# Performance work log

Measured on AMD Instinct MI355X. Metric: run time of the kernel, lower is better.

## Reference

```python
import jax, jax.numpy as jnp
import numpy as np

B, S, D, DQKV = 4, 2048, 1024, 1024

def setup_inputs() -> dict:
    key = jax.random.key(0)
    kx, kq, kk, kv = jax.random.split(key, 4)
    scale = 1.0 / np.sqrt(D)
    return {
        "x": jax.random.normal(kx, (B, S, D), dtype=jnp.float32),
        "wq": jax.random.normal(kq, (D, DQKV), dtype=jnp.float32) * scale,
        "wk": jax.random.normal(kk, (D, DQKV), dtype=jnp.float32) * scale,
        "wv": jax.random.normal(kv, (D, DQKV), dtype=jnp.float32) * scale,
    }

def reference(x, wq, wk, wv):
    # QKV projections: [B,S,D] @ [D,Dqkv] -> [B,S,Dqkv]
    q = jnp.einsum('bsd,de->bse', x, wq)
    k = jnp.einsum('bsd,de->bse', x, wk)
    v = jnp.einsum('bsd,de->bse', x, wv)
    # scores: [B,S,S], scaled by sqrt(dim_qkv)
    scores = jnp.einsum('bik,bjk->bij', q, k) / jnp.sqrt(jnp.asarray(DQKV, dtype=x.dtype))
    attn = jax.nn.softmax(scores, axis=-1)
    # output: [B,S,Dqkv]
    return jnp.einsum('bij,bjd->bid', attn, v)
```

## Files before the change

kernel.cpp:

```cpp
#include <hip/hip_runtime.h>
#include <cstdint>
#include <cstddef>

typedef __bf16 bf16;
typedef __bf16 bf16x4 __attribute__((ext_vector_type(4)));
typedef __bf16 bf16x8 __attribute__((ext_vector_type(8)));
typedef float  f32x4  __attribute__((ext_vector_type(4)));
typedef float  f32x16 __attribute__((ext_vector_type(16)));

#define BATCH 4
#define SEQ   2048
#define DIM   1024
#define LDP   2112

__device__ __forceinline__ bf16 to_bf16(float f) {
    unsigned u = __builtin_bit_cast(unsigned, f);
    u += 0x7fffu + ((u >> 16) & 1u);
    unsigned short h = (unsigned short)(u >> 16);
    return __builtin_bit_cast(bf16, h);
}

__device__ __forceinline__ void load16_lds(const bf16* g, bf16* l) {
    __builtin_amdgcn_global_load_lds(
        (__attribute__((address_space(1))) void*)(g),
        (__attribute__((address_space(3))) void*)(l),
        16, 0, 0);
}

#define BARRIER() do { asm volatile("" ::: "memory"); \
                       __builtin_amdgcn_s_barrier();  \
                       asm volatile("" ::: "memory"); } while (0)
#define LGKM0()   asm volatile("s_waitcnt lgkmcnt(0)" ::: "memory")
#define VM4()     asm volatile("s_waitcnt vmcnt(4)" ::: "memory")
#define VM0()     asm volatile("s_waitcnt vmcnt(0)" ::: "memory")


__device__ __forceinline__ void stage_half(
    const bf16* __restrict__ srcRow0, int ld, int k0, bf16* dstHalfBase)
{
    const int tid  = threadIdx.x;
    const int wave = tid >> 6;
    const int lane = tid & 63;
    const int rg   = lane >> 3;
    const int scoff = ((lane & 7) ^ rg) * 8;
#pragma unroll
    for (int j = 0; j < 2; ++j) {
        const int r = wave * 16 + j * 8;
        load16_lds(srcRow0 + (size_t)(r + rg) * ld + k0 + scoff,
                   dstHalfBase + r * 64);
    }
}

template<int MB, int NB>
__device__ __forceinline__ void mfma_quad(
    const bf16x8 a[4][2], const bf16x8 b[4][2], f32x4 acc[8][4])
{
    __builtin_amdgcn_s_setprio(1);
#pragma unroll
    for (int m = 0; m < 4; ++m)
#pragma unroll
        for (int n = 0; n < 2; ++n)
#pragma unroll
            for (int ks = 0; ks < 2; ++ks)
                acc[MB + m][NB + n] = __builtin_amdgcn_mfma_f32_16x16x32_bf16(
                    a[m][ks], b[NB + n][ks], acc[MB + m][NB + n], 0, 0, 0);
    __builtin_amdgcn_s_setprio(0);
}

__device__ __forceinline__ void gemm8_core(
    const bf16* __restrict__ Ablk, const bf16* __restrict__ Bblk,
    int K, int lda, int ldb, bf16* As, bf16* Bs, f32x4 acc[8][4])
{
    const int tid  = threadIdx.x;
    const int lane = tid & 63;
    const int wave = tid >> 6;
    const int wr   = wave >> 2;
    const int wc   = wave & 3;
    const int r16  = lane & 15;
    const int g    = lane >> 4;
    const int r7   = r16 & 7;
    const int pk0  = ((g) ^ r7) * 8;
    const int pk1  = ((4 + g) ^ r7) * 8;
    const int arow = (wr * 128 + r16) * 64;
    const int brow = (wc * 64 + r16) * 64;
    const int NT   = K >> 6;

    stage_half(Bblk, ldb, 0, Bs);
    stage_half(Ablk, lda, 0, As);
    stage_half(Bblk + (size_t)128 * ldb, ldb, 0, Bs + 8192);
    stage_half(Ablk + (size_t)128 * lda, lda, 0, As + 8192);
    stage_half(Bblk, ldb, 64, Bs + 16384);
    stage_half(Ablk, lda, 64, As + 16384);
    VM4();
    BARRIER();

    bf16x8 a[4][2], b[4][2];
#pragma unroll 2
    for (int t = 0; t < NT; ++t) {
        bf16* Ac = As + (t & 1) * 16384;
        bf16* Bc = Bs + (t & 1) * 16384;
        bf16* An = As + ((t + 1) & 1) * 16384;
        bf16* Bn = Bs + ((t + 1) & 1) * 16384;
        const int k1 = (t + 1) << 6;
        const int k2 = (t + 2) << 6;

#pragma unroll
        for (int m = 0; m < 4; ++m) {
            a[m][0] = *(const bf16x8*)(Ac + arow + m * 1024 + pk0);
            a[m][1] = *(const bf16x8*)(Ac + arow + m * 1024 + pk1);
        }
#pragma unroll
        for (int n = 0; n < 2; ++n) {
            b[n][0] = *(const bf16x8*)(Bc + brow + n * 1024 + pk0);
            b[n][1] = *(const bf16x8*)(Bc + brow + n * 1024 + pk1);
        }
        if (t + 1 < NT) stage_half(Bblk + (size_t)128 * ldb, ldb, k1, Bn + 8192);
        BARRIER(); LGKM0();
        mfma_quad<0, 0>(a, b, acc);
        BARRIER();

#pragma unroll
        for (int n = 2; n < 4; ++n) {
            b[n][0] = *(const bf16x8*)(Bc + brow + n * 1024 + pk0);
            b[n][1] = *(const bf16x8*)(Bc + brow + n * 1024 + pk1);
        }
        if (t + 1 < NT) stage_half(Ablk + (size_t)128 * lda, lda, k1, An + 8192);
        BARRIER(); LGKM0();
        mfma_quad<0, 2>(a, b, acc);
        BARRIER();

#pragma unroll
        for (int m = 0; m < 4; ++m) {
            a[m][0] = *(const bf16x8*)(Ac + arow + 4096 + m * 1024 + pk0);
            a[m][1] = *(const bf16x8*)(Ac + arow + 4096 + m * 1024 + pk1);
        }
        if (t + 2 < NT) stage_half(Bblk, ldb, k2, Bc);
        BARRIER(); LGKM0();
        mfma_quad<4, 2>(a, b, acc);
        BARRIER();

        if (t + 2 < NT) stage_half(Ablk, lda, k2, Ac);
        BARRIER(); LGKM0();
        mfma_quad<4, 0>(a, b, acc);
        if (t + 1 < NT) {
            if (t + 2 < NT) { VM4(); } else { VM0(); }
        }
        BARRIER();
    }
}

__device__ __forceinline__ void stage_tiles(
    const bf16* __restrict__ Abase, const bf16* __restrict__ Bbase,
    int k0, int lda, int ldb, bf16* As, bf16* Bs)
{
    const int tid   = threadIdx.x;
    const int wave  = tid >> 6;
    const int lane  = tid & 63;
    const int srow0 = wave * 8 + (lane >> 3);
    const int scoff = (((lane & 7) ^ ((lane >> 3) & 7)) * 8);
    const int ldsW  = wave * 512;
#pragma unroll
    for (int j = 0; j < 4; ++j) {
        load16_lds(Abase + (size_t)(j * 32 + srow0) * lda + k0 + scoff,
                   As + j * 2048 + ldsW);
        load16_lds(Bbase + (size_t)(j * 32 + srow0) * ldb + k0 + scoff,
                   Bs + j * 2048 + ldsW);
    }
}

__device__ __forceinline__ void gemm_core64_32(
    const bf16* __restrict__ Abase, const bf16* __restrict__ Bbase,
    int K, int lda, int ldb, bf16* As, bf16* Bs, f32x16 acc[2][2])
{
    const int tid  = threadIdx.x;
    const int lane = tid & 63;
    const int wave = tid >> 6;
    const int wm   = (wave >> 1) * 64;
    const int wn   = (wave & 1) * 64;
    const int r32  = lane & 31;
    const int hi   = lane >> 5;

    for (int k0 = 0; k0 < K; k0 += 64) {
        __syncthreads();
        stage_tiles(Abase, Bbase, k0, lda, ldb, As, Bs);
        __syncthreads();
#pragma unroll
        for (int t = 0; t < 4; ++t) {
            bf16x8 af[2], bfr[2];
            const int p = (2 * t + hi) ^ (r32 & 7);
#pragma unroll
            for (int i = 0; i < 2; ++i) {
                af[i]  = *(const bf16x8*)(As + (wm + i * 32 + r32) * 64 + p * 8);
                bfr[i] = *(const bf16x8*)(Bs + (wn + i * 32 + r32) * 64 + p * 8);
            }
#pragma unroll
            for (int mi = 0; mi < 2; ++mi)
#pragma unroll
                for (int ni = 0; ni < 2; ++ni)
                    acc[mi][ni] = __builtin_amdgcn_mfma_f32_32x32x16_bf16(
                        af[mi], bfr[ni], acc[mi][ni], 0, 0, 0);
        }
    }
}

__device__ __forceinline__ int c32_row(int reg, int hi) {
    return (reg & 3) + 8 * (reg >> 2) + 4 * hi;
}

__global__ __launch_bounds__(512, 2) void proj_gemm8(
    const bf16* __restrict__ xb, const bf16* __restrict__ Wt,
    bf16* __restrict__ Q, bf16* __restrict__ Kb, bf16* __restrict__ Vt)
{
    __shared__ bf16 As[32768];
    __shared__ bf16 Bs[32768];
    f32x4 acc[8][4] = {};

    const int r = blockIdx.x;
    const bf16 *Ab, *Bb;
    bf16* Cb;
    int ldc;
    if (r < 256) {
        const int my = r >> 3, j = r & 7;
        Ab = xb + (size_t)my * 256 * DIM;
        Bb = Wt + (size_t)((j >> 2) ? DIM * DIM : 0) + (size_t)(j & 3) * 256 * DIM;
        bf16* dst = (j >> 2) ? Kb : Q;
        Cb = dst + (size_t)my * 256 * DIM + (size_t)(j & 3) * 256;
        ldc = DIM;
    } else {
        const int u = r - 256;
        const int bz = u >> 5, w = u & 31;
        const int vy = w >> 3, vx = w & 7;
        Ab = Wt + (size_t)2 * DIM * DIM + (size_t)vy * 256 * DIM;
        Bb = xb + (size_t)bz * SEQ * DIM + (size_t)vx * 256 * DIM;
        Cb = Vt + (size_t)bz * DIM * LDP + (size_t)vy * 256 * LDP + (size_t)vx * 256;
        ldc = LDP;
    }
    gemm8_core(Ab, Bb, DIM, DIM, DIM, As, Bs, acc);

    const int lane = threadIdx.x & 63;
    const int wave = threadIdx.x >> 6;
    const int wr = wave >> 2, wc = wave & 3;
    const int r16 = lane & 15, g = lane >> 4;
    const int row0 = wr * 128 + g * 4;
    const int col0 = wc * 64 + r16;
#pragma unroll
    for (int m = 0; m < 8; ++m)
#pragma unroll
        for (int n = 0; n < 4; ++n)
#pragma unroll
            for (int rr = 0; rr < 4; ++rr)
                Cb[(size_t)(row0 + m * 16 + rr) * ldc + col0 + n * 16] =
                    to_bf16(acc[m][n][rr]);
}

__global__ __launch_bounds__(512, 2) void gemm_scores8(
    const bf16* __restrict__ Qm, const bf16* __restrict__ Kb,
    bf16* __restrict__ P, float* __restrict__ lsum)
{
    __shared__ bf16 As[32768];
    __shared__ bf16 Bs[32768];
    f32x4 acc[8][4] = {};

    const int d = blockIdx.x;
    const int bx = d & 7, by = (d >> 3) & 7, bz = d >> 6;
    const bf16* Ab = Qm + (size_t)bz * SEQ * DIM + (size_t)by * 256 * DIM;
    const bf16* Bb = Kb + (size_t)bz * SEQ * DIM + (size_t)bx * 256 * DIM;
    gemm8_core(Ab, Bb, DIM, DIM, DIM, As, Bs, acc);

    bf16* Cb  = P + (size_t)bz * SEQ * LDP;
    float* ls = lsum + (size_t)bz * SEQ;
    const int lane = threadIdx.x & 63;
    const int wave = threadIdx.x >> 6;
    const int wr = wave >> 2, wc = wave & 3;
    const int r16 = lane & 15, g = lane >> 4;
    const int rowB = by * 256 + wr * 128 + g * 4;
    const int colB = bx * 256 + wc * 64 + r16;
#pragma unroll
    for (int m = 0; m < 8; ++m)
#pragma unroll
        for (int rr = 0; rr < 4; ++rr) {
            float s = 0.0f;
#pragma unroll
            for (int n = 0; n < 4; ++n) {
                const float e = __expf(acc[m][n][rr] * 0.03125f);
                s += e;
                Cb[(size_t)(rowB + m * 16 + rr) * LDP + colB + n * 16] = to_bf16(e);
            }
            s += __shfl_xor(s, 1);
            s += __shfl_xor(s, 2);
            s += __shfl_xor(s, 4);
            s += __shfl_xor(s, 8);
            if (r16 == 0)
                atomicAdd(ls + rowB + m * 16 + rr, s);
        }
}

__global__ __launch_bounds__(256, 4) void gemm_pv(
    const bf16* __restrict__ P, const bf16* __restrict__ Vt, float* __restrict__ C,
    const float* __restrict__ lsum)
{
    __shared__ bf16 As[8192];
    __shared__ bf16 Bs[8192];
    f32x16 acc[2][2] = {};

    const int d = blockIdx.x + 8 * (blockIdx.y + 16 * blockIdx.z);
    const int c = d & 7, j = d >> 3;
    const int bx = j & 7;
    const int p = c + 8 * (j >> 3);
    const int by = p & 15, bz = p >> 4;

    const bf16* Ab = P  + (size_t)bz * SEQ * LDP + (size_t)by * 128 * LDP;
    const bf16* Bb = Vt + (size_t)bz * DIM * LDP + (size_t)bx * 128 * LDP;
    float* Cb = C + (size_t)bz * SEQ * DIM;
    gemm_core64_32(Ab, Bb, SEQ, LDP, LDP, As, Bs, acc);

    const int lane = threadIdx.x & 63;
    const int wave = threadIdx.x >> 6;
    const int hi = lane >> 5, r32 = lane & 31;
    const int wm = (wave >> 1) * 64, wn = (wave & 1) * 64;
    const int rowBase = by * 128 + wm;
    const int colBase = bx * 128 + wn + r32;
    const float* ls = lsum + (size_t)bz * SEQ;
#pragma unroll
    for (int mi = 0; mi < 2; ++mi)
#pragma unroll
        for (int reg = 0; reg < 16; ++reg) {
            const int row = rowBase + mi * 32 + c32_row(reg, hi);
            const float inv = __builtin_amdgcn_rcpf(ls[row]);
#pragma unroll
            for (int ni = 0; ni < 2; ++ni)
                Cb[(size_t)row * DIM + colBase + ni * 32] = acc[mi][ni][reg] * inv;
        }
}

__global__ __launch_bounds__(256) void prep(
    const float* __restrict__ x,  const float* __restrict__ wq,
    const float* __restrict__ wk, const float* __restrict__ wv,
    bf16* __restrict__ xb, bf16* __restrict__ Wt, float* __restrict__ lsum)
{
    __shared__ float tile[32][33];
    const int b = blockIdx.x;
    const int tid = threadIdx.x;
    if (b < 8192) {
        const size_t i = ((size_t)b * 256 + tid) * 4;
        const float4 v = *(const float4*)(x + i);
        bf16x4 o = { to_bf16(v.x), to_bf16(v.y), to_bf16(v.z), to_bf16(v.w) };
        *(bf16x4*)(xb + i) = o;
    } else if (b < 8192 + 3072) {
        const int t   = b - 8192;
        const int sel = t >> 10;
        const int n0  = (t & 31) * 32;
        const int k0  = ((t >> 5) & 31) * 32;
        const float* w = (sel == 0) ? wq : (sel == 1) ? wk : wv;
        const int tx = tid & 31, ty = tid >> 5;
#pragma unroll
        for (int j = 0; j < 32; j += 8)
            tile[ty + j][tx] = w[(size_t)(k0 + ty + j) * 1024 + n0 + tx];
        __syncthreads();
        bf16* dst = Wt + (size_t)sel * 1024 * 1024;
#pragma unroll
        for (int j = 0; j < 32; j += 8)
            dst[(size_t)(n0 + ty + j) * 1024 + k0 + tx] = to_bf16(tile[tx][ty + j]);
    } else {
#pragma unroll
        for (int i = 0; i < 32; ++i)
            lsum[i * 256 + tid] = 0.0f;
    }
}

extern "C" void kernel_launch(void* const* d_in, const int* in_sizes, int n_in,
                              void* d_out, int out_size, void* d_ws, size_t ws_size,
                              hipStream_t stream)
{
    const float* x  = (const float*)d_in[0];
    const float* wq = (const float*)d_in[1];
    const float* wk = (const float*)d_in[2];
    const float* wv = (const float*)d_in[3];
    float* out = (float*)d_out;
    char* ws = (char*)d_ws;

    bf16*  xb   = (bf16*)(ws);
    bf16*  Wt   = (bf16*)(ws + (16u << 20));
    bf16*  Q    = (bf16*)(ws + (22u << 20));
    bf16*  Kb   = (bf16*)(ws + (38u << 20));
    bf16*  Vt   = (bf16*)(ws + (54u << 20));
    bf16*  P    = (bf16*)(ws + (72u << 20));
    float* lsum = (float*)(ws + (108u << 20));

    prep<<<dim3(8192 + 3072 + 1), dim3(256), 0, stream>>>(
        x, wq, wk, wv, xb, Wt, lsum);

    proj_gemm8<<<dim3(384), dim3(512), 0, stream>>>(xb, Wt, Q, Kb, Vt);

    gemm_scores8<<<dim3(256), dim3(512), 0, stream>>>(Q, Kb, P, lsum);

    gemm_pv<<<dim3(8, 16, 4), dim3(256), 0, stream>>>(P, Vt, out, lsum);
}
```

Baseline: 245.8 us.

## Replace 8-wave ping-pong GEMM schedule with simple double-buffered loop, split projection launch

```diff
diff --git a/kernel.cpp b/kernel.cpp
--- a/kernel.cpp
+++ b/kernel.cpp
@@ -31,7 +31,6 @@
                        __builtin_amdgcn_s_barrier();  \
                        asm volatile("" ::: "memory"); } while (0)
 #define LGKM0()   asm volatile("s_waitcnt lgkmcnt(0)" ::: "memory")
-#define VM4()     asm volatile("s_waitcnt vmcnt(4)" ::: "memory")
 #define VM0()     asm volatile("s_waitcnt vmcnt(0)" ::: "memory")
 
 
@@ -51,23 +50,7 @@
     }
 }
 
-template<int MB, int NB>
-__device__ __forceinline__ void mfma_quad(
-    const bf16x8 a[4][2], const bf16x8 b[4][2], f32x4 acc[8][4])
-{
-    __builtin_amdgcn_s_setprio(1);
-#pragma unroll
-    for (int m = 0; m < 4; ++m)
-#pragma unroll
-        for (int n = 0; n < 2; ++n)
-#pragma unroll
-            for (int ks = 0; ks < 2; ++ks)
-                acc[MB + m][NB + n] = __builtin_amdgcn_mfma_f32_16x16x32_bf16(
-                    a[m][ks], b[NB + n][ks], acc[MB + m][NB + n], 0, 0, 0);
-    __builtin_amdgcn_s_setprio(0);
-}
-
-__device__ __forceinline__ void gemm8_core(
+__device__ __forceinline__ void gemm_big_core(
     const bf16* __restrict__ Ablk, const bf16* __restrict__ Bblk,
     int K, int lda, int ldb, bf16* As, bf16* Bs, f32x4 acc[8][4])
 {
@@ -86,15 +69,12 @@
     const int NT   = K >> 6;
 
     stage_half(Bblk, ldb, 0, Bs);
+    stage_half(Bblk + (size_t)128 * ldb, ldb, 0, Bs + 8192);
     stage_half(Ablk, lda, 0, As);
-    stage_half(Bblk + (size_t)128 * ldb, ldb, 0, Bs + 8192);
     stage_half(Ablk + (size_t)128 * lda, lda, 0, As + 8192);
-    stage_half(Bblk, ldb, 64, Bs + 16384);
-    stage_half(Ablk, lda, 64, As + 16384);
-    VM4();
+    VM0();
     BARRIER();
 
-    bf16x8 a[4][2], b[4][2];
 #pragma unroll 2
     for (int t = 0; t < NT; ++t) {
         bf16* Ac = As + (t & 1) * 16384;
@@ -102,51 +82,69 @@
         bf16* An = As + ((t + 1) & 1) * 16384;
         bf16* Bn = Bs + ((t + 1) & 1) * 16384;
         const int k1 = (t + 1) << 6;
-        const int k2 = (t + 2) << 6;
-
+
+        bf16x8 b[4][2], a[4][2], a2[4][2];
+#pragma unroll
+        for (int n = 0; n < 4; ++n) {
+            b[n][0] = *(const bf16x8*)(Bc + brow + n * 1024 + pk0);
+            b[n][1] = *(const bf16x8*)(Bc + brow + n * 1024 + pk1);
+        }
 #pragma unroll
         for (int m = 0; m < 4; ++m) {
             a[m][0] = *(const bf16x8*)(Ac + arow + m * 1024 + pk0);
             a[m][1] = *(const bf16x8*)(Ac + arow + m * 1024 + pk1);
         }
-#pragma unroll
-        for (int n = 0; n < 2; ++n) {
-            b[n][0] = *(const bf16x8*)(Bc + brow + n * 1024 + pk0);
-            b[n][1] = *(const bf16x8*)(Bc + brow + n * 1024 + pk1);
-        }
-        if (t + 1 < NT) stage_half(Bblk + (size_t)128 * ldb, ldb, k1, Bn + 8192);
-        BARRIER(); LGKM0();
-        mfma_quad<0, 0>(a, b, acc);
+        if (t + 1 < NT) {
+            stage_half(Bblk, ldb, k1, Bn);
+            stage_half(Bblk + (size_t)128 * ldb, ldb, k1, Bn + 8192);
+            stage_half(Ablk, lda, k1, An);
+            stage_half(Ablk + (size_t)128 * lda, lda, k1, An + 8192);
+        }
+#pragma unroll
+        for (int m = 0; m < 4; ++m)
+#pragma unroll
+            for (int n = 0; n < 4; ++n)
+#pragma unroll
+                for (int ks = 0; ks < 2; ++ks)
+                    acc[m][n] = __builtin_amdgcn_mfma_f32_16x16x32_bf16(
+                        a[m][ks], b[n][ks], acc[m][n], 0, 0, 0);
+#pragma unroll
+        for (int m = 0; m < 4; ++m) {
+            a2[m][0] = *(const bf16x8*)(Ac + arow + 4096 + m * 1024 + pk0);
+            a2[m][1] = *(const bf16x8*)(Ac + arow + 4096 + m * 1024 + pk1);
+        }
+#pragma unroll
+        for (int m = 0; m < 4; ++m)
+#pragma unroll
+            for (int n = 0; n < 4; ++n)
+#pragma unroll
+                for (int ks = 0; ks < 2; ++ks)
+                    acc[4 + m][n] = __builtin_amdgcn_mfma_f32_16x16x32_bf16(
+                        a2[m][ks], b[n][ks], acc[4 + m][n], 0, 0, 0);
+
+        LGKM0();
+        if (t + 1 < NT) VM0();
         BARRIER();
-
-#pragma unroll
-        for (int n = 2; n < 4; ++n) {
-            b[n][0] = *(const bf16x8*)(Bc + brow + n * 1024 + pk0);
-            b[n][1] = *(const bf16x8*)(Bc + brow + n * 1024 + pk1);
-        }
-        if (t + 1 < NT) stage_half(Ablk + (size_t)128 * lda, lda, k1, An + 8192);
-        BARRIER(); LGKM0();
-        mfma_quad<0, 2>(a, b, acc);
-        BARRIER();
-
-#pragma unroll
-        for (int m = 0; m < 4; ++m) {
-            a[m][0] = *(const bf16x8*)(Ac + arow + 4096 + m * 1024 + pk0);
-            a[m][1] = *(const bf16x8*)(Ac + arow + 4096 + m * 1024 + pk1);
-        }
-        if (t + 2 < NT) stage_half(Bblk, ldb, k2, Bc);
-        BARRIER(); LGKM0();
-        mfma_quad<4, 2>(a, b, acc);
-        BARRIER();
-
-        if (t + 2 < NT) stage_half(Ablk, lda, k2, Ac);
-        BARRIER(); LGKM0();
-        mfma_quad<4, 0>(a, b, acc);
-        if (t + 1 < NT) {
-            if (t + 2 < NT) { VM4(); } else { VM0(); }
-        }
-        BARRIER();
-    }
+    }
+}
+
+__device__ __forceinline__ void write_c256(
+    bf16* __restrict__ Cb, int ldc, const f32x4 acc[8][4])
+{
+    const int lane = threadIdx.x & 63;
+    const int wave = threadIdx.x >> 6;
+    const int wr = wave >> 2, wc = wave & 3;
+    const int r16 = lane & 15, g = lane >> 4;
+    const int row0 = wr * 128 + g * 4;
+    const int col0 = wc * 64 + r16;
+#pragma unroll
+    for (int m = 0; m < 8; ++m)
+#pragma unroll
+        for (int n = 0; n < 4; ++n)
+#pragma unroll
+            for (int rr = 0; rr < 4; ++rr)
+                Cb[(size_t)(row0 + m * 16 + rr) * ldc + col0 + n * 16] =
+                    to_bf16(acc[m][n][rr]);
 }
 
 __device__ __forceinline__ void stage_tiles(
@@ -207,50 +205,44 @@
     return (reg & 3) + 8 * (reg >> 2) + 4 * hi;
 }
 
-__global__ __launch_bounds__(512, 2) void proj_gemm8(
+__global__ __launch_bounds__(512, 2) void proj_qk(
     const bf16* __restrict__ xb, const bf16* __restrict__ Wt,
-    bf16* __restrict__ Q, bf16* __restrict__ Kb, bf16* __restrict__ Vt)
+    bf16* __restrict__ Q, bf16* __restrict__ Kb)
 {
     __shared__ bf16 As[32768];
     __shared__ bf16 Bs[32768];
     f32x4 acc[8][4] = {};
 
     const int r = blockIdx.x;
-    const bf16 *Ab, *Bb;
-    bf16* Cb;
-    int ldc;
-    if (r < 256) {
-        const int my = r >> 3, j = r & 7;
-        Ab = xb + (size_t)my * 256 * DIM;
-        Bb = Wt + (size_t)((j >> 2) ? DIM * DIM : 0) + (size_t)(j & 3) * 256 * DIM;
-        bf16* dst = (j >> 2) ? Kb : Q;
-        Cb = dst + (size_t)my * 256 * DIM + (size_t)(j & 3) * 256;
-        ldc = DIM;
-    } else {
-        const int u = r - 256;
-        const int bz = u >> 5, w = u & 31;
-        const int vy = w >> 3, vx = w & 7;
-        Ab = Wt + (size_t)2 * DIM * DIM + (size_t)vy * 256 * DIM;
-        Bb = xb + (size_t)bz * SEQ * DIM + (size_t)vx * 256 * DIM;
-        Cb = Vt + (size_t)bz * DIM * LDP + (size_t)vy * 256 * LDP + (size_t)vx * 256;
-        ldc = LDP;
-    }
-    gemm8_core(Ab, Bb, DIM, DIM, DIM, As, Bs, acc);
-
-    const int lane = threadIdx.x & 63;
-    const int wave = threadIdx.x >> 6;
-    const int wr = wave >> 2, wc = wave & 3;
-    const int r16 = lane & 15, g = lane >> 4;
-    const int row0 = wr * 128 + g * 4;
-    const int col0 = wc * 64 + r16;
-#pragma unroll
-    for (int m = 0; m < 8; ++m)
-#pragma unroll
-        for (int n = 0; n < 4; ++n)
-#pragma unroll
-            for (int rr = 0; rr < 4; ++rr)
-                Cb[(size_t)(row0 + m * 16 + rr) * ldc + col0 + n * 16] =
-                    to_bf16(acc[m][n][rr]);
+    const int my = r >> 3, j = r & 7;
+    const bf16* Ab = xb + (size_t)my * 256 * DIM;
+    const bf16* Bb = Wt + (size_t)((j >> 2) ? DIM * DIM : 0)
+                        + (size_t)(j & 3) * 256 * DIM;
+    bf16* dst = (j >> 2) ? Kb : Q;
+    bf16* Cb = dst + (size_t)my * 256 * DIM + (size_t)(j & 3) * 256;
+
+    gemm_big_core(Ab, Bb, DIM, DIM, DIM, As, Bs, acc);
+    write_c256(Cb, DIM, acc);
+}
+
+__global__ __launch_bounds__(512, 2) void proj_v(
+    const bf16* __restrict__ xb, const bf16* __restrict__ Wt,
+    bf16* __restrict__ Vt)
+{
+    __shared__ bf16 As[32768];
+    __shared__ bf16 Bs[32768];
+    f32x4 acc[8][4] = {};
+
+    const int u = blockIdx.x;
+    const int bz = u >> 5, w = u & 31;
+    const int vy = w >> 3, vx = w & 7;
+    const bf16* Ab = Wt + (size_t)2 * DIM * DIM + (size_t)vy * 256 * DIM;
+    const bf16* Bb = xb + (size_t)bz * SEQ * DIM + (size_t)vx * 256 * DIM;
+    bf16* Cb = Vt + (size_t)bz * DIM * LDP + (size_t)vy * 256 * LDP
+                  + (size_t)vx * 256;
+
+    gemm_big_core(Ab, Bb, DIM, DIM, DIM, As, Bs, acc);
+    write_c256(Cb, LDP, acc);
 }
 
 __global__ __launch_bounds__(512, 2) void gemm_scores8(
@@ -265,7 +257,7 @@
     const int bx = d & 7, by = (d >> 3) & 7, bz = d >> 6;
     const bf16* Ab = Qm + (size_t)bz * SEQ * DIM + (size_t)by * 256 * DIM;
     const bf16* Bb = Kb + (size_t)bz * SEQ * DIM + (size_t)bx * 256 * DIM;
-    gemm8_core(Ab, Bb, DIM, DIM, DIM, As, Bs, acc);
+    gemm_big_core(Ab, Bb, DIM, DIM, DIM, As, Bs, acc);
 
     bf16* Cb  = P + (size_t)bz * SEQ * LDP;
     float* ls = lsum + (size_t)bz * SEQ;
@@ -390,7 +382,8 @@
     prep<<<dim3(8192 + 3072 + 1), dim3(256), 0, stream>>>(
         x, wq, wk, wv, xb, Wt, lsum);
 
-    proj_gemm8<<<dim3(384), dim3(512), 0, stream>>>(xb, Wt, Q, Kb, Vt);
+    proj_qk<<<dim3(256), dim3(512), 0, stream>>>(xb, Wt, Q, Kb);
+    proj_v<<<dim3(128), dim3(512), 0, stream>>>(xb, Wt, Vt);
 
     gemm_scores8<<<dim3(256), dim3(512), 0, stream>>>(Q, Kb, P, lsum);
 
```

Measured after the change: 233.7 us. -4.9%, faster.
